# Kernel optimization log

Measured on AMD Instinct MI355X. Metric: run time of the kernel, lower is better.

## Reference

```python
import jax, jax.numpy as jnp
import numpy as np
from jax import lax

BS, L, H = 8, 2048, 1024
NH, HD = 16, 64


def setup_inputs() -> dict:
    key = jax.random.key(0)
    ks = jax.random.split(key, 4)
    s = 1.0 / np.sqrt(H)
    xav = np.sqrt(2.0 / (NH + HD))  # xavier_normal_ for ReadingHead (fan_in=HD? torch uses dims (NH,HD))
    return {
        "hidden_states": jax.random.normal(ks[0], (BS, L, H), jnp.float32),
        "K1_w": jax.random.normal(ks[1], (H, NH * HD), jnp.float32) * s,
        "K1_b": jnp.zeros((NH * HD,), jnp.float32),
        "V1_w": jax.random.normal(ks[2], (H, NH * HD), jnp.float32) * s,
        "V1_b": jnp.zeros((NH * HD,), jnp.float32),
        "bidirection_weight": jnp.full((1, 1, NH, 1, 4), 0.25, jnp.float32),
        "ReadingHead": jax.random.normal(ks[3], (NH, HD), jnp.float32) * xav,
    }


def _nearest_valid_maps(valid, L):
    # valid: [bs, L, nh] bool. Returns fm, bm: [bs, L, 2, nh] int32, matching the
    # original sequential torch loop (including its use of len_index = L-1-j for the
    # backward map's slot 0).
    bs, _, nh = valid.shape
    mask_t = jnp.moveaxis(valid, 1, 0)  # [L, bs, nh]

    def step(carry, x):
        a, b = carry
        m, v = x
        nb = jnp.where(m, a, b)
        na = jnp.where(m, v, a)
        return (na, nb), (na, nb)

    zero = jnp.zeros((bs, nh), jnp.int32)
    idx_fwd = jnp.arange(1, L, dtype=jnp.int32)
    _, (fa, fb) = lax.scan(step, (zero, zero), (mask_t[1:], idx_fwd))
    fa = jnp.concatenate([zero[None], fa], axis=0)  # [L, bs, nh]
    fb = jnp.concatenate([zero[None], fb], axis=0)

    last = jnp.full((bs, nh), L - 1, jnp.int32)
    # backward loop stores len_index = L-1-j at position j when valid
    vals_bwd = (L - 1) - jnp.arange(L - 1, dtype=jnp.int32)
    _, (ba, bb) = lax.scan(step, (last, last), (mask_t[: L - 1], vals_bwd), reverse=True)
    ba = jnp.concatenate([ba, last[None]], axis=0)
    bb = jnp.concatenate([bb, last[None]], axis=0)

    fm = jnp.stack([fa, fb], axis=2).transpose(1, 0, 2, 3)  # [bs, L, 2, nh]
    bm = jnp.stack([ba, bb], axis=2).transpose(1, 0, 2, 3)
    return fm, bm


def reference(hidden_states, K1_w, K1_b, V1_w, V1_b, bidirection_weight, ReadingHead):
    bs, length, _ = hidden_states.shape
    nh, hd = ReadingHead.shape
    K1 = jax.nn.relu(hidden_states @ K1_w + K1_b).reshape(bs, length, nh, hd)
    V1 = jax.nn.relu(hidden_states @ V1_w + V1_b).reshape(bs, length, nh, hd)
    dots = jnp.einsum('blnh,nh->bln', K1, ReadingHead)
    valid = dots > 0.5
    fm, bm = _nearest_valid_maps(valid, length)
    # gather V along sequence dim with the two nearest-valid maps
    Vf = jnp.take_along_axis(V1, fm.reshape(bs, 2 * length, nh, 1), axis=1)
    Vf = Vf.reshape(bs, length, 2, nh, hd)
    Vb = jnp.take_along_axis(V1, bm.reshape(bs, 2 * length, nh, 1), axis=1)
    Vb = Vb.reshape(bs, length, 2, nh, hd)
    # [bs, L, 4, nh, hd] -> [bs, L, nh, hd, 4], weighted sum over the 4 registers
    new_states = jnp.concatenate([Vf, Vb], axis=2).transpose(0, 1, 3, 4, 2) * bidirection_weight
    context = new_states.sum(axis=-1).reshape(bs, length, nh * hd)
    return context
```

## Files before the change

kernel.cpp:

```cpp
#include <hip/hip_runtime.h>
#include <hip/hip_bf16.h>
#include <cstdint>

#define BS 8
#define SEQ 2048
#define HDIM 1024
#define NH 16
#define HD 64
#define M_ROWS (BS * SEQ)
#define N_COLS (2 * HDIM)
#define KDIM HDIM

#define DELTA 0.025f
#define FLAG_CAP 32768

#define OFF_A      ((size_t)0)
#define OFF_BT     ((size_t)33554432)
#define OFF_FCNT   ((size_t)37748736)
#define OFF_FLIST  ((size_t)37748800)
#define OFF_BIAS   ((size_t)38273088)
#define OFF_CV     ((size_t)41943040)
#define OFF_VALID  ((size_t)109051904)
#define OFF_MAPS   ((size_t)109314048)

typedef __attribute__((ext_vector_type(8))) __bf16 bf16x8;
typedef __attribute__((ext_vector_type(4))) float f32x4;

__device__ __forceinline__ unsigned short f2bf(float f) {
    unsigned int x = __builtin_bit_cast(unsigned int, f);
    unsigned int r = x + 0x7fffu + ((x >> 16) & 1u);
    return (unsigned short)(r >> 16);
}

__device__ __forceinline__ void g2l16(const void* gp, void* lp) {
    __builtin_amdgcn_global_load_lds(
        (__attribute__((address_space(1))) void*)(void*)gp,
        (__attribute__((address_space(3))) void*)lp, 16, 0, 0);
}

__global__ __launch_bounds__(256) void cvt_hs_kernel(const float4* __restrict__ in,
                                                     ushort4* __restrict__ outp) {
    int i = blockIdx.x * 256 + threadIdx.x;
    float4 v = in[i];
    ushort4 o;
    o.x = f2bf(v.x); o.y = f2bf(v.y); o.z = f2bf(v.z); o.w = f2bf(v.w);
    outp[i] = o;
}

__global__ __launch_bounds__(256) void cvt_w_kernel(const float* __restrict__ K1w,
                                                    const float* __restrict__ V1w,
                                                    unsigned short* __restrict__ Bt) {
    __shared__ float tile[32][33];
    const float* W = blockIdx.z ? V1w : K1w;
    int tn = blockIdx.x, tk = blockIdx.y;
    int t = threadIdx.x;
    int r = t >> 3;
    int c4 = (t & 7) * 4;
    const float4 v = *(const float4*)&W[(size_t)(tk * 32 + r) * 1024 + tn * 32 + c4];
    tile[r][c4 + 0] = v.x; tile[r][c4 + 1] = v.y; tile[r][c4 + 2] = v.z; tile[r][c4 + 3] = v.w;
    __syncthreads();
    int n = tn * 32 + r;
    int k = tk * 32 + c4;
    float f0 = tile[c4 + 0][r], f1 = tile[c4 + 1][r], f2 = tile[c4 + 2][r], f3 = tile[c4 + 3][r];
    size_t obase = ((size_t)blockIdx.z * 1024 + n) * 1024 + k;
    ushort4 o; o.x = f2bf(f0); o.y = f2bf(f1); o.z = f2bf(f2); o.w = f2bf(f3);
    *(ushort4*)&Bt[obase] = o;
}

__global__ void cvt_bias_kernel(const float* __restrict__ K1b, const float* __restrict__ V1b,
                                float* __restrict__ bias, int* __restrict__ fcnt) {
    int i = blockIdx.x * 256 + threadIdx.x;
    bias[i] = (i < 1024) ? K1b[i] : V1b[i - 1024];
    if (i == 0) *fcnt = 0;
}

__global__ __launch_bounds__(256) void gemm_kernel(const unsigned short* __restrict__ Abf,
                                                   const unsigned short* __restrict__ Btbf,
                                                   const float* __restrict__ bias,
                                                   const float* __restrict__ RH,
                                                   float* __restrict__ CV,
                                                   unsigned char* __restrict__ valid,
                                                   int* __restrict__ fcnt,
                                                   int* __restrict__ flist) {
    constexpr int K = KDIM, BK = 32;
    __shared__ unsigned short As[128 * BK];
    __shared__ unsigned short Bs[128 * BK];
    const int t = threadIdx.x;
    const int wave = t >> 6, lane = t & 63;
    const int wm = wave >> 1, wn = wave & 1;
    const int l16 = lane & 15, quad = lane >> 4;
    const int m0 = blockIdx.y * 128, n0 = blockIdx.x * 128;

    f32x4 zero4 = {0.f, 0.f, 0.f, 0.f};
    f32x4 acc[4][4];
#pragma unroll
    for (int i = 0; i < 4; i++)
#pragma unroll
        for (int j = 0; j < 4; j++) acc[i][j] = zero4;

    const int srow = t >> 2;
    const int sk = (t & 3) * 8;
    const unsigned short* gA = Abf + (size_t)(m0 + srow) * K + sk;
    const unsigned short* gB = Btbf + (size_t)(n0 + srow) * K + sk;
    char* lAs = (char*)As + (size_t)wave * 1024;
    char* lBs = (char*)Bs + (size_t)wave * 1024;

    for (int k0 = 0; k0 < K; k0 += BK) {
        g2l16(gA + k0, lAs);
        g2l16(gA + (size_t)64 * K + k0, lAs + 4096);
        g2l16(gB + k0, lBs);
        g2l16(gB + (size_t)64 * K + k0, lBs + 4096);
        __syncthreads();
        bf16x8 af[4], bfr[4];
#pragma unroll
        for (int mt = 0; mt < 4; mt++)
            af[mt] = *(const bf16x8*)&As[(wm * 64 + mt * 16 + l16) * BK + quad * 8];
#pragma unroll
        for (int nt = 0; nt < 4; nt++)
            bfr[nt] = *(const bf16x8*)&Bs[(wn * 64 + nt * 16 + l16) * BK + quad * 8];
#pragma unroll
        for (int mt = 0; mt < 4; mt++)
#pragma unroll
            for (int nt = 0; nt < 4; nt++)
                acc[mt][nt] = __builtin_amdgcn_mfma_f32_16x16x32_bf16(af[mt], bfr[nt], acc[mt][nt], 0, 0, 0);
        __syncthreads();
    }
    if (n0 < HDIM) {
        const int n = (n0 >> 6) + wn;
        float rh[4], bv[4];
#pragma unroll
        for (int nt = 0; nt < 4; nt++) {
            int col = n * 64 + nt * 16 + l16;
            rh[nt] = RH[col];
            bv[nt] = bias[col];
        }
#pragma unroll
        for (int mt = 0; mt < 4; mt++) {
#pragma unroll
            for (int r = 0; r < 4; r++) {
                float p = 0.f;
#pragma unroll
                for (int nt = 0; nt < 4; nt++)
                    p += fmaxf(acc[mt][nt][r] + bv[nt], 0.f) * rh[nt];
#pragma unroll
                for (int s = 8; s >= 1; s >>= 1) p += __shfl_xor(p, s, 64);
                if (l16 == 0) {
                    int row = m0 + wm * 64 + mt * 16 + quad * 4 + r;
                    int b = row >> 11, l = row & (SEQ - 1);
                    valid[((size_t)b * NH + n) * SEQ + l] = (p > 0.5f) ? 1 : 0;
                    if (fabsf(p - 0.5f) < DELTA) {
                        int idx = atomicAdd(fcnt, 1);
                        if (idx < FLAG_CAP) flist[idx] = row * NH + n;
                    }
                }
            }
        }
    } else {
        const int nv0 = n0 - HDIM;
#pragma unroll
        for (int mt = 0; mt < 4; mt++) {
            int gm = m0 + wm * 64 + mt * 16 + quad * 4;
#pragma unroll
            for (int nt = 0; nt < 4; nt++) {
                int gn = nv0 + wn * 64 + nt * 16 + l16;
                float bvv = bias[HDIM + gn];
#pragma unroll
                for (int r = 0; r < 4; r++)
                    CV[(size_t)(gm + r) * HDIM + gn] = fmaxf(acc[mt][nt][r] + bvv, 0.f);
            }
        }
    }
}

__global__ __launch_bounds__(256) void refine_kernel(const float* __restrict__ hs,
                                                     const float* __restrict__ K1w,
                                                     const float* __restrict__ K1b,
                                                     const float* __restrict__ RH,
                                                     const int* __restrict__ fcnt,
                                                     const int* __restrict__ flist,
                                                     unsigned char* __restrict__ valid) {
    int cnt = *fcnt;
    if (cnt > FLAG_CAP) cnt = FLAG_CAP;
    const int wave = threadIdx.x >> 6, d = threadIdx.x & 63;
    const int task = blockIdx.x * 4 + wave;
    if (task >= cnt) return;

    const int code = flist[task];
    const int n = code & (NH - 1);
    const int bl = code >> 4;
    const float* x = hs + (size_t)bl * HDIM;
    const float* wp = K1w + n * 64 + d;

    double acc0 = 0.0, acc1 = 0.0, acc2 = 0.0, acc3 = 0.0;
    for (int k = 0; k < KDIM; k += 32) {
        float w[32];
#pragma unroll
        for (int u = 0; u < 32; u++)
            w[u] = wp[(size_t)(k + u) * 1024];
        float4 xv[8];
#pragma unroll
        for (int u = 0; u < 8; u++)
            xv[u] = *(const float4*)(x + k + u * 4);
#pragma unroll
        for (int u = 0; u < 8; u++) {
            acc0 += (double)xv[u].x * (double)w[u * 4 + 0];
            acc1 += (double)xv[u].y * (double)w[u * 4 + 1];
            acc2 += (double)xv[u].z * (double)w[u * 4 + 2];
            acc3 += (double)xv[u].w * (double)w[u * 4 + 3];
        }
    }
    double k1 = ((acc0 + acc1) + (acc2 + acc3)) + (double)K1b[n * 64 + d];
    if (k1 < 0.0) k1 = 0.0;
    double contrib = k1 * (double)RH[n * 64 + d];
#pragma unroll
    for (int s = 32; s >= 1; s >>= 1) contrib += __shfl_xor(contrib, s, 64);
    if (d == 0) {
        int b = bl >> 11, l = bl & (SEQ - 1);
        valid[((size_t)b * NH + n) * SEQ + l] = (contrib > 0.5) ? 1 : 0;
    }
}

__global__ __launch_bounds__(64) void scan_kernel(const unsigned char* __restrict__ valid,
                                                  ushort4* __restrict__ maps) {
    int bn = blockIdx.x;
    int b = bn >> 4, n = bn & (NH - 1);
    int lane = threadIdx.x;
    __shared__ unsigned int summ[64];

    const unsigned char* vp = valid + (size_t)bn * SEQ + lane * 32;
    uint4 c0 = *(const uint4*)vp;
    uint4 c1 = *(const uint4*)(vp + 16);
    unsigned int wds[8] = {c0.x, c0.y, c0.z, c0.w, c1.x, c1.y, c1.z, c1.w};
    unsigned int mask = 0;
#pragma unroll
    for (int i = 0; i < 8; i++) {
#pragma unroll
        for (int j = 0; j < 4; j++)
            mask |= (((wds[i] >> (8 * j)) & 0xffu) ? 1u : 0u) << (i * 4 + j);
    }

    int cnt = 0, va = 0, vb = 0;
#pragma unroll
    for (int tt = 0; tt < 32; tt++) {
        if (mask & (1u << tt)) { vb = va; va = lane * 32 + tt; cnt++; }
    }
    summ[lane] = (unsigned)((cnt > 2 ? 2 : cnt) | (va << 2) | (vb << 13));
    __syncthreads();
    int a = 0, bb_ = 0;
    for (int tt = 0; tt < lane; tt++) {
        unsigned s = summ[tt];
        int c = s & 3, sva = (s >> 2) & 2047, svb = (s >> 13) & 2047;
        if (c >= 2) { a = sva; bb_ = svb; }
        else if (c == 1) { bb_ = a; a = sva; }
    }
    unsigned int fres[32];
#pragma unroll
    for (int tt = 0; tt < 32; tt++) {
        if (mask & (1u << tt)) { bb_ = a; a = lane * 32 + tt; }
        fres[tt] = (unsigned)a | ((unsigned)bb_ << 16);
    }
    __syncthreads();

    unsigned int maskb = mask;
    if (lane == 63) maskb &= ~(1u << 31);
    cnt = 0; va = 0; vb = 0;
#pragma unroll
    for (int tt = 31; tt >= 0; tt--) {
        if (maskb & (1u << tt)) { vb = va; va = (SEQ - 1) - (lane * 32 + tt); cnt++; }
    }
    summ[lane] = (unsigned)((cnt > 2 ? 2 : cnt) | (va << 2) | (vb << 13));
    __syncthreads();
    int a2 = SEQ - 1, b2 = SEQ - 1;
    for (int tt = 63; tt > lane; tt--) {
        unsigned s = summ[tt];
        int c = s & 3, sva = (s >> 2) & 2047, svb = (s >> 13) & 2047;
        if (c >= 2) { a2 = sva; b2 = svb; }
        else if (c == 1) { b2 = a2; a2 = sva; }
    }
#pragma unroll
    for (int tt = 31; tt >= 0; tt--) {
        int j = lane * 32 + tt;
        if (maskb & (1u << tt)) { b2 = a2; a2 = (SEQ - 1) - j; }
        unsigned f = fres[tt];
        maps[((size_t)b * SEQ + j) * NH + n] =
            make_ushort4((unsigned short)(f & 0xffffu), (unsigned short)(f >> 16),
                         (unsigned short)a2, (unsigned short)b2);
    }
}

__global__ __launch_bounds__(256) void gather_kernel(const float* __restrict__ CV,
                                                     const ushort4* __restrict__ maps,
                                                     const float* __restrict__ bw,
                                                     float* __restrict__ out) {
    int bl = blockIdx.x;
    int t = threadIdx.x, n = t >> 4, q = t & 15;
    int b = bl >> 11;
    ushort4 m = maps[(size_t)bl * NH + n];
    const float4 w = *(const float4*)&bw[n * 4];
    size_t colbase = (size_t)(n * 64 + q * 4);
    size_t rowb = (size_t)b * SEQ;
    const float4 v0 = *(const float4*)&CV[(rowb + m.x) * HDIM + colbase];
    const float4 v1 = *(const float4*)&CV[(rowb + m.y) * HDIM + colbase];
    const float4 v2 = *(const float4*)&CV[(rowb + m.z) * HDIM + colbase];
    const float4 v3 = *(const float4*)&CV[(rowb + m.w) * HDIM + colbase];
    float4 o;
    o.x = w.x * v0.x + w.y * v1.x + w.z * v2.x + w.w * v3.x;
    o.y = w.x * v0.y + w.y * v1.y + w.z * v2.y + w.w * v3.y;
    o.z = w.x * v0.z + w.y * v1.z + w.z * v2.z + w.w * v3.z;
    o.w = w.x * v0.w + w.y * v1.w + w.z * v2.w + w.w * v3.w;
    *(float4*)&out[(size_t)bl * (NH * HD) + n * 64 + q * 4] = o;
}

extern "C" void kernel_launch(void* const* d_in, const int* in_sizes, int n_in,
                              void* d_out, int out_size, void* d_ws, size_t ws_size,
                              hipStream_t stream) {
    (void)in_sizes; (void)n_in; (void)out_size; (void)ws_size;
    const float* hs  = (const float*)d_in[0];
    const float* K1w = (const float*)d_in[1];
    const float* K1b = (const float*)d_in[2];
    const float* V1w = (const float*)d_in[3];
    const float* V1b = (const float*)d_in[4];
    const float* bw  = (const float*)d_in[5];
    const float* RH  = (const float*)d_in[6];
    float* out = (float*)d_out;
    char* ws = (char*)d_ws;

    unsigned short* Abf  = (unsigned short*)(ws + OFF_A);
    unsigned short* Btbf = (unsigned short*)(ws + OFF_BT);
    int* fcnt = (int*)(ws + OFF_FCNT);
    int* flist = (int*)(ws + OFF_FLIST);
    float* bias  = (float*)(ws + OFF_BIAS);
    float* CV    = (float*)(ws + OFF_CV);
    unsigned char* valid = (unsigned char*)(ws + OFF_VALID);
    ushort4* maps = (ushort4*)(ws + OFF_MAPS);

    cvt_bias_kernel<<<8, 256, 0, stream>>>(K1b, V1b, bias, fcnt);
    cvt_hs_kernel<<<16384, 256, 0, stream>>>((const float4*)hs, (ushort4*)Abf);
    cvt_w_kernel<<<dim3(32, 32, 2), 256, 0, stream>>>(K1w, V1w, Btbf);
    gemm_kernel<<<dim3(N_COLS / 128, M_ROWS / 128), 256, 0, stream>>>(
        Abf, Btbf, bias, RH, CV, valid, fcnt, flist);
    refine_kernel<<<FLAG_CAP / 4, 256, 0, stream>>>(
        hs, K1w, K1b, RH, fcnt, flist, valid);
    scan_kernel<<<BS * NH, 64, 0, stream>>>(valid, maps);
    gather_kernel<<<BS * SEQ, 256, 0, stream>>>(CV, maps, bw, out);
}
```

Before: 411.1 us.

## Store V in bf16, widen GEMM K-tile with swizzled LDS, fuse prep kernels

Three changes. First, the three conversion kernels (hidden states, weights, bias) are merged into one launch. Second, the GEMM K-tile grows from 32 to 64, with an XOR swizzle on the LDS layout to avoid bank conflicts. Third, the V projection is stored as bf16 instead of fp32, halving its write and gather traffic. This adds extra rounding of V, which may reduce output accuracy.

```diff
diff --git a/kernel.cpp b/kernel.cpp
--- a/kernel.cpp
+++ b/kernel.cpp
@@ -18,10 +18,10 @@
 #define OFF_BT     ((size_t)33554432)
 #define OFF_FCNT   ((size_t)37748736)
 #define OFF_FLIST  ((size_t)37748800)
-#define OFF_BIAS   ((size_t)38273088)
-#define OFF_CV     ((size_t)41943040)
-#define OFF_VALID  ((size_t)109051904)
-#define OFF_MAPS   ((size_t)109314048)
+#define OFF_BIAS   ((size_t)37879872)
+#define OFF_CVH    ((size_t)41943040)
+#define OFF_VALID  ((size_t)75497472)
+#define OFF_MAPS   ((size_t)75759616)
 
 typedef __attribute__((ext_vector_type(8))) __bf16 bf16x8;
 typedef __attribute__((ext_vector_type(4))) float f32x4;
@@ -31,6 +31,9 @@
     unsigned int r = x + 0x7fffu + ((x >> 16) & 1u);
     return (unsigned short)(r >> 16);
 }
+__device__ __forceinline__ float bf2f(unsigned short u) {
+    return __builtin_bit_cast(float, (unsigned int)u << 16);
+}
 
 __device__ __forceinline__ void g2l16(const void* gp, void* lp) {
     __builtin_amdgcn_global_load_lds(
@@ -38,57 +41,65 @@
         (__attribute__((address_space(3))) void*)lp, 16, 0, 0);
 }
 
-__global__ __launch_bounds__(256) void cvt_hs_kernel(const float4* __restrict__ in,
-                                                     ushort4* __restrict__ outp) {
-    int i = blockIdx.x * 256 + threadIdx.x;
-    float4 v = in[i];
-    ushort4 o;
-    o.x = f2bf(v.x); o.y = f2bf(v.y); o.z = f2bf(v.z); o.w = f2bf(v.w);
-    outp[i] = o;
-}
-
-__global__ __launch_bounds__(256) void cvt_w_kernel(const float* __restrict__ K1w,
-                                                    const float* __restrict__ V1w,
-                                                    unsigned short* __restrict__ Bt) {
+__global__ __launch_bounds__(256) void prep_kernel(const float4* __restrict__ hs4,
+                                                   ushort4* __restrict__ Abf4,
+                                                   const float* __restrict__ K1w,
+                                                   const float* __restrict__ V1w,
+                                                   unsigned short* __restrict__ Bt,
+                                                   const float* __restrict__ K1b,
+                                                   const float* __restrict__ V1b,
+                                                   float* __restrict__ bias,
+                                                   int* __restrict__ fcnt) {
     __shared__ float tile[32][33];
-    const float* W = blockIdx.z ? V1w : K1w;
-    int tn = blockIdx.x, tk = blockIdx.y;
-    int t = threadIdx.x;
-    int r = t >> 3;
-    int c4 = (t & 7) * 4;
-    const float4 v = *(const float4*)&W[(size_t)(tk * 32 + r) * 1024 + tn * 32 + c4];
-    tile[r][c4 + 0] = v.x; tile[r][c4 + 1] = v.y; tile[r][c4 + 2] = v.z; tile[r][c4 + 3] = v.w;
-    __syncthreads();
-    int n = tn * 32 + r;
-    int k = tk * 32 + c4;
-    float f0 = tile[c4 + 0][r], f1 = tile[c4 + 1][r], f2 = tile[c4 + 2][r], f3 = tile[c4 + 3][r];
-    size_t obase = ((size_t)blockIdx.z * 1024 + n) * 1024 + k;
-    ushort4 o; o.x = f2bf(f0); o.y = f2bf(f1); o.z = f2bf(f2); o.w = f2bf(f3);
-    *(ushort4*)&Bt[obase] = o;
-}
-
-__global__ void cvt_bias_kernel(const float* __restrict__ K1b, const float* __restrict__ V1b,
-                                float* __restrict__ bias, int* __restrict__ fcnt) {
-    int i = blockIdx.x * 256 + threadIdx.x;
-    bias[i] = (i < 1024) ? K1b[i] : V1b[i - 1024];
-    if (i == 0) *fcnt = 0;
+    const int blk = blockIdx.x;
+    const int t = threadIdx.x;
+    if (blk < 16384) {
+        int i = blk * 256 + t;
+        float4 v = hs4[i];
+        ushort4 o;
+        o.x = f2bf(v.x); o.y = f2bf(v.y); o.z = f2bf(v.z); o.w = f2bf(v.w);
+        Abf4[i] = o;
+    } else if (blk < 18432) {
+        int lb = blk - 16384;
+        int z = lb >> 10;
+        int tk = (lb >> 5) & 31;
+        int tn = lb & 31;
+        const float* W = z ? V1w : K1w;
+        int r = t >> 3;
+        int c4 = (t & 7) * 4;
+        const float4 v = *(const float4*)&W[(size_t)(tk * 32 + r) * 1024 + tn * 32 + c4];
+        tile[r][c4 + 0] = v.x; tile[r][c4 + 1] = v.y;
+        tile[r][c4 + 2] = v.z; tile[r][c4 + 3] = v.w;
+        __syncthreads();
+        int n = tn * 32 + r;
+        int k = tk * 32 + c4;
+        ushort4 o;
+        o.x = f2bf(tile[c4 + 0][r]); o.y = f2bf(tile[c4 + 1][r]);
+        o.z = f2bf(tile[c4 + 2][r]); o.w = f2bf(tile[c4 + 3][r]);
+        *(ushort4*)&Bt[((size_t)z * 1024 + n) * 1024 + k] = o;
+    } else {
+        int i = (blk - 18432) * 256 + t;
+        bias[i] = (i < 1024) ? K1b[i] : V1b[i - 1024];
+        if (i == 0) *fcnt = 0;
+    }
 }
 
 __global__ __launch_bounds__(256) void gemm_kernel(const unsigned short* __restrict__ Abf,
                                                    const unsigned short* __restrict__ Btbf,
                                                    const float* __restrict__ bias,
                                                    const float* __restrict__ RH,
-                                                   float* __restrict__ CV,
+                                                   unsigned short* __restrict__ CVh,
                                                    unsigned char* __restrict__ valid,
                                                    int* __restrict__ fcnt,
                                                    int* __restrict__ flist) {
-    constexpr int K = KDIM, BK = 32;
+    constexpr int K = KDIM, BK = 64;
     __shared__ unsigned short As[128 * BK];
     __shared__ unsigned short Bs[128 * BK];
     const int t = threadIdx.x;
     const int wave = t >> 6, lane = t & 63;
     const int wm = wave >> 1, wn = wave & 1;
     const int l16 = lane & 15, quad = lane >> 4;
+    const int sw = l16 & 7;
     const int m0 = blockIdx.y * 128, n0 = blockIdx.x * 128;
 
     f32x4 zero4 = {0.f, 0.f, 0.f, 0.f};
@@ -98,31 +109,37 @@
 #pragma unroll
         for (int j = 0; j < 4; j++) acc[i][j] = zero4;
 
-    const int srow = t >> 2;
-    const int sk = (t & 3) * 8;
-    const unsigned short* gA = Abf + (size_t)(m0 + srow) * K + sk;
-    const unsigned short* gB = Btbf + (size_t)(n0 + srow) * K + sk;
+    const int rr = t >> 3;
+    const int gsw = (t ^ (t >> 3)) & 7;
+    const unsigned short* gA = Abf + (size_t)(m0 + rr) * K + gsw * 8;
+    const unsigned short* gB = Btbf + (size_t)(n0 + rr) * K + gsw * 8;
     char* lAs = (char*)As + (size_t)wave * 1024;
     char* lBs = (char*)Bs + (size_t)wave * 1024;
 
     for (int k0 = 0; k0 < K; k0 += BK) {
-        g2l16(gA + k0, lAs);
-        g2l16(gA + (size_t)64 * K + k0, lAs + 4096);
-        g2l16(gB + k0, lBs);
-        g2l16(gB + (size_t)64 * K + k0, lBs + 4096);
+#pragma unroll
+        for (int i = 0; i < 4; i++)
+            g2l16(gA + (size_t)i * 32 * K + k0, lAs + i * 4096);
+#pragma unroll
+        for (int i = 0; i < 4; i++)
+            g2l16(gB + (size_t)i * 32 * K + k0, lBs + i * 4096);
         __syncthreads();
-        bf16x8 af[4], bfr[4];
-#pragma unroll
-        for (int mt = 0; mt < 4; mt++)
-            af[mt] = *(const bf16x8*)&As[(wm * 64 + mt * 16 + l16) * BK + quad * 8];
-#pragma unroll
-        for (int nt = 0; nt < 4; nt++)
-            bfr[nt] = *(const bf16x8*)&Bs[(wn * 64 + nt * 16 + l16) * BK + quad * 8];
-#pragma unroll
-        for (int mt = 0; mt < 4; mt++)
+#pragma unroll
+        for (int h = 0; h < 2; h++) {
+            bf16x8 af[4], bfr[4];
+            const int hq = h * 4 + quad;
+#pragma unroll
+            for (int mt = 0; mt < 4; mt++)
+                af[mt] = *(const bf16x8*)&As[(wm * 64 + mt * 16 + l16) * BK + (hq ^ sw) * 8];
 #pragma unroll
             for (int nt = 0; nt < 4; nt++)
-                acc[mt][nt] = __builtin_amdgcn_mfma_f32_16x16x32_bf16(af[mt], bfr[nt], acc[mt][nt], 0, 0, 0);
+                bfr[nt] = *(const bf16x8*)&Bs[(wn * 64 + nt * 16 + l16) * BK + (hq ^ sw) * 8];
+#pragma unroll
+            for (int mt = 0; mt < 4; mt++)
+#pragma unroll
+                for (int nt = 0; nt < 4; nt++)
+                    acc[mt][nt] = __builtin_amdgcn_mfma_f32_16x16x32_bf16(af[mt], bfr[nt], acc[mt][nt], 0, 0, 0);
+        }
         __syncthreads();
     }
     if (n0 < HDIM) {
@@ -166,7 +183,7 @@
                 float bvv = bias[HDIM + gn];
 #pragma unroll
                 for (int r = 0; r < 4; r++)
-                    CV[(size_t)(gm + r) * HDIM + gn] = fmaxf(acc[mt][nt][r] + bvv, 0.f);
+                    CVh[(size_t)(gm + r) * HDIM + gn] = f2bf(fmaxf(acc[mt][nt][r] + bvv, 0.f));
             }
         }
     }
@@ -288,7 +305,7 @@
     }
 }
 
-__global__ __launch_bounds__(256) void gather_kernel(const float* __restrict__ CV,
+__global__ __launch_bounds__(256) void gather_kernel(const unsigned short* __restrict__ CVh,
                                                      const ushort4* __restrict__ maps,
                                                      const float* __restrict__ bw,
                                                      float* __restrict__ out) {
@@ -299,15 +316,15 @@
     const float4 w = *(const float4*)&bw[n * 4];
     size_t colbase = (size_t)(n * 64 + q * 4);
     size_t rowb = (size_t)b * SEQ;
-    const float4 v0 = *(const float4*)&CV[(rowb + m.x) * HDIM + colbase];
-    const float4 v1 = *(const float4*)&CV[(rowb + m.y) * HDIM + colbase];
-    const float4 v2 = *(const float4*)&CV[(rowb + m.z) * HDIM + colbase];
-    const float4 v3 = *(const float4*)&CV[(rowb + m.w) * HDIM + colbase];
+    const ushort4 u0 = *(const ushort4*)&CVh[(rowb + m.x) * HDIM + colbase];
+    const ushort4 u1 = *(const ushort4*)&CVh[(rowb + m.y) * HDIM + colbase];
+    const ushort4 u2 = *(const ushort4*)&CVh[(rowb + m.z) * HDIM + colbase];
+    const ushort4 u3 = *(const ushort4*)&CVh[(rowb + m.w) * HDIM + colbase];
     float4 o;
-    o.x = w.x * v0.x + w.y * v1.x + w.z * v2.x + w.w * v3.x;
-    o.y = w.x * v0.y + w.y * v1.y + w.z * v2.y + w.w * v3.y;
-    o.z = w.x * v0.z + w.y * v1.z + w.z * v2.z + w.w * v3.z;
-    o.w = w.x * v0.w + w.y * v1.w + w.z * v2.w + w.w * v3.w;
+    o.x = w.x * bf2f(u0.x) + w.y * bf2f(u1.x) + w.z * bf2f(u2.x) + w.w * bf2f(u3.x);
+    o.y = w.x * bf2f(u0.y) + w.y * bf2f(u1.y) + w.z * bf2f(u2.y) + w.w * bf2f(u3.y);
+    o.z = w.x * bf2f(u0.z) + w.y * bf2f(u1.z) + w.z * bf2f(u2.z) + w.w * bf2f(u3.z);
+    o.w = w.x * bf2f(u0.w) + w.y * bf2f(u1.w) + w.z * bf2f(u2.w) + w.w * bf2f(u3.w);
     *(float4*)&out[(size_t)bl * (NH * HD) + n * 64 + q * 4] = o;
 }
 
@@ -330,17 +347,16 @@
     int* fcnt = (int*)(ws + OFF_FCNT);
     int* flist = (int*)(ws + OFF_FLIST);
     float* bias  = (float*)(ws + OFF_BIAS);
-    float* CV    = (float*)(ws + OFF_CV);
+    unsigned short* CVh = (unsigned short*)(ws + OFF_CVH);
     unsigned char* valid = (unsigned char*)(ws + OFF_VALID);
     ushort4* maps = (ushort4*)(ws + OFF_MAPS);
 
-    cvt_bias_kernel<<<8, 256, 0, stream>>>(K1b, V1b, bias, fcnt);
-    cvt_hs_kernel<<<16384, 256, 0, stream>>>((const float4*)hs, (ushort4*)Abf);
-    cvt_w_kernel<<<dim3(32, 32, 2), 256, 0, stream>>>(K1w, V1w, Btbf);
+    prep_kernel<<<18440, 256, 0, stream>>>((const float4*)hs, (ushort4*)Abf,
+                                           K1w, V1w, Btbf, K1b, V1b, bias, fcnt);
     gemm_kernel<<<dim3(N_COLS / 128, M_ROWS / 128), 256, 0, stream>>>(
-        Abf, Btbf, bias, RH, CV, valid, fcnt, flist);
+        Abf, Btbf, bias, RH, CVh, valid, fcnt, flist);
     refine_kernel<<<FLAG_CAP / 4, 256, 0, stream>>>(
         hs, K1w, K1b, RH, fcnt, flist, valid);
     scan_kernel<<<BS * NH, 64, 0, stream>>>(valid, maps);
-    gather_kernel<<<BS * SEQ, 256, 0, stream>>>(CV, maps, bw, out);
-}
+    gather_kernel<<<BS * SEQ, 256, 0, stream>>>(CVh, maps, bw, out);
+}
```

New measurement: 375.1 us. 1.1x faster.
